# Kernel tuning notes

Measured on AMD Instinct MI355X. Metric: run time of the kernel, lower is better.

The kernel has to match this reference:

```python
import jax, jax.numpy as jnp
import numpy as np

K = 3        # kernel_size
GROUP = 32   # group
EPS = 1e-5   # BatchNorm eps


def setup_inputs() -> dict:
    key = jax.random.key(0)
    k1, k2 = jax.random.split(key)
    x = jax.random.normal(k1, (4, 256, 128, 128), jnp.float32)
    conv_w = jax.random.normal(k2, (GROUP * K * K, 256, K, K), jnp.float32) * 0.05
    gamma = jnp.ones((GROUP * K * K,), jnp.float32)
    beta = jnp.zeros((GROUP * K * K,), jnp.float32)
    return {"x": x, "conv_w": conv_w, "gamma": gamma, "beta": beta}


def _bilinear_align_corners(x, H, W):
    # F.upsample(..., mode='bilinear', align_corners=True)
    n, c, h, w = x.shape
    ys = jnp.linspace(0.0, h - 1.0, H)
    xs = jnp.linspace(0.0, w - 1.0, W)
    y0 = jnp.floor(ys).astype(jnp.int32)
    x0 = jnp.floor(xs).astype(jnp.int32)
    y1 = jnp.minimum(y0 + 1, h - 1)
    x1 = jnp.minimum(x0 + 1, w - 1)
    wy = (ys - y0)[None, None, :, None]
    wx = (xs - x0)[None, None, None, :]
    rows0 = x[:, :, y0, :]
    rows1 = x[:, :, y1, :]
    top = rows0[:, :, :, x0] * (1 - wx) + rows0[:, :, :, x1] * wx
    bot = rows1[:, :, :, x0] * (1 - wx) + rows1[:, :, :, x1] * wx
    return top * (1 - wy) + bot * wy


def reference(x, conv_w, gamma, beta):
    n, c, h0, w0 = x.shape
    # sigma = softmax(BN(conv(x))) over the full G*K*K channel dim
    sigma = jax.lax.conv_general_dilated(
        x, conv_w, (1, 1), 'VALID', dimension_numbers=('NCHW', 'OIHW', 'NCHW'))
    mean = sigma.mean(axis=(0, 2, 3))
    var = sigma.var(axis=(0, 2, 3))  # biased, matches BN training mode
    sigma = (sigma - mean[None, :, None, None]) * jax.lax.rsqrt(var + EPS)[None, :, None, None]
    sigma = sigma * gamma[None, :, None, None] + beta[None, :, None, None]
    sigma = jax.nn.softmax(sigma, axis=1)  # (n, G*K*K, h, w)
    h, w = sigma.shape[2], sigma.shape[3]  # h = h0-K+1, w = w0-K+1
    # Unfold: patches (n, c, K*K, h, w) with channel outer, kernel-pos inner (torch F.unfold order)
    patches = jnp.stack([x[:, :, i:i + h, j:j + w]
                         for i in range(K) for j in range(K)], axis=2)
    patches = patches.reshape(n, GROUP, c // GROUP, K * K, h, w)
    sig = sigma.reshape(n, GROUP, K * K, h, w)
    # Per-pixel, per-group weighted sum over the K*K window
    out = jnp.einsum('ngcphw,ngphw->ngchw', patches, sig).reshape(n, c, h, w)
    return _bilinear_align_corners(out, h0, w0)
```

## Files before the change

### kernel.cpp

```cpp
#include <hip/hip_runtime.h>
#include <hip/hip_bf16.h>
#include <math.h>

#define N 4
#define C 256
#define H 128
#define W 128
#define CO 288
#define OH 126
#define OW 126
#define GROUP 32
#define CPG 8
#define EPS 1e-5f

#define HW (OH*OW)
#define XSLICE (H*W)
#define XNSTRIDE (C*H*W)
#define SNSTRIDE (CO*HW)
#define LONSTRIDE (C*HW)
#define WSTRIDE (CO*256)
#define WTOT (9*CO*256)
#define XTOT (N*H*W*C)

typedef unsigned short u16;
typedef __attribute__((ext_vector_type(8))) short short8;
typedef __attribute__((ext_vector_type(4))) float float4v;

__device__ inline u16 f2bf(float v) {
    __hip_bfloat16 b = __float2bfloat16(v);
    return __builtin_bit_cast(u16, b);
}
__device__ inline float bf2f(u16 u) {
    __hip_bfloat16 b = __builtin_bit_cast(__hip_bfloat16, u);
    return __bfloat162float(b);
}

__global__ __launch_bounds__(256) void split_x_kernel(const float* __restrict__ x,
                                                      u16* __restrict__ xh,
                                                      u16* __restrict__ xl) {
    const int ci = threadIdx.x;
    const int w0 = blockIdx.x * 8;
    const int h  = blockIdx.y;
    const int n  = blockIdx.z;
    const float* src = x + ((size_t)(n*C + ci)*H + h)*W + w0;
    float4 v0 = *(const float4*)src;
    float4 v1 = *(const float4*)(src + 4);
    float vals[8] = {v0.x, v0.y, v0.z, v0.w, v1.x, v1.y, v1.z, v1.w};
    size_t obase = ((size_t)(n*H + h)*W + w0)*C + ci;
    #pragma unroll
    for (int dw = 0; dw < 8; ++dw) {
        float v = vals[dw];
        u16 hb = f2bf(v);
        xh[obase + (size_t)dw*C] = hb;
        xl[obase + (size_t)dw*C] = f2bf(v - bf2f(hb));
    }
}

__global__ __launch_bounds__(256) void split_w_kernel(const float* __restrict__ wgt,
                                                      u16* __restrict__ whT,
                                                      u16* __restrict__ wlT) {
    const int i = blockIdx.x*256 + threadIdx.x;
    const int ci = i & 255;
    const int co = (i >> 8) % CO;
    const int s  = i / (CO*256);
    float v = wgt[(size_t)co*(C*9) + (size_t)ci*9 + s];
    u16 hb = f2bf(v);
    whT[i] = hb;
    wlT[i] = f2bf(v - bf2f(hb));
}

__global__ __launch_bounds__(512, 2) void conv_mfma_kernel(const u16* __restrict__ xh,
                                                           const u16* __restrict__ whT,
                                                           float* __restrict__ sigma) {
    __shared__ __align__(16) u16 xs[25600];
    __shared__ __align__(16) u16 wsh[2*18432];

    const int tid  = threadIdx.x;
    const int wave = tid >> 6;
    const int lane = tid & 63;
    const int m16  = lane & 15;
    const int q    = lane >> 4;
    const int wr   = wave & 3;
    const int wc   = wave >> 2;
    const int ow0  = blockIdx.x * 64;
    const int oh0  = blockIdx.y * 4;
    const int n    = blockIdx.z;

    const int w_n    = (wave < 4) ? 5 : 4;
    const int w_base = (wave < 4) ? wave*320 : 1280 + (wave-4)*256;
    int wsrc[5];
    #pragma unroll
    for (int i = 0; i < 5; ++i) {
        int c = w_base + i*64 + lane;
        const int sp  = c / 1152;
        const int rem = c - sp*1152;
        const int qc  = rem / 288;
        const int co  = rem - qc*288;
        wsrc[i] = sp*WTOT + co*256 + qc*8;
    }

    int xoff[7];
    #pragma unroll
    for (int t = 0; t < 7; ++t) {
        int c = (8*t + wave)*64 + lane;
        if (c > 3167) c = 3167;
        const int spq = c / 396;
        const int rem = c - spq*396;
        const int row = rem / 66;
        const int col = rem - row*66;
        int gr = oh0 + row; if (gr > H-1) gr = H-1;
        int gc = ow0 + col; if (gc > W-1) gc = W-1;
        xoff[t] = (spq >> 2)*XTOT + ((n*H + gr)*W + gc)*C + (spq & 3)*8;
    }

    const int aoff = (q*396 + wr*66 + m16)*8;
    const int boff = (q*288 + wc*144 + m16)*8;

    float4v acc[4][9];
    #pragma unroll
    for (int mt = 0; mt < 4; ++mt)
        #pragma unroll
        for (int j = 0; j < 9; ++j) acc[mt][j] = (float4v)(0.f);

    #pragma unroll
    for (int t = 0; t < 7; ++t)
        if (t < 6 || wave < 2)
            __builtin_amdgcn_global_load_lds((const uint*)(xh + xoff[t]),
                                             (uint*)(xs + (8*t + wave)*512), 16, 0, 0);
    #pragma unroll
    for (int i = 0; i < 5; ++i)
        if (i < w_n)
            __builtin_amdgcn_global_load_lds((const uint*)(whT + wsrc[i]),
                                             (uint*)(wsh + (w_base + i*64)*8), 16, 0, 0);
    __syncthreads();

    int buf = 0;
    for (int ci0 = 0; ci0 < C; ci0 += 32) {
        #pragma unroll 1
        for (int s = 0; s < 9; ++s) {
            if (s < 8) {
                const int soff = (s+1)*WSTRIDE + ci0;
                #pragma unroll
                for (int i = 0; i < 5; ++i)
                    if (i < w_n)
                        __builtin_amdgcn_global_load_lds(
                            (const uint*)(whT + soff + wsrc[i]),
                            (uint*)(wsh + ((buf^1)*18432 + (w_base + i*64)*8)), 16, 0, 0);
            }

            const int ky = s / 3;
            const int kx = s - 3*ky;
            const int ab = aoff + (ky*66 + kx)*8;
            short8 ah0 = *(const short8*)&xs[ab];
            short8 ah1 = *(const short8*)&xs[ab + 128];
            short8 ah2 = *(const short8*)&xs[ab + 256];
            short8 ah3 = *(const short8*)&xs[ab + 384];
            short8 al0 = *(const short8*)&xs[ab + 12672];
            short8 al1 = *(const short8*)&xs[ab + 12672 + 128];
            short8 al2 = *(const short8*)&xs[ab + 12672 + 256];
            short8 al3 = *(const short8*)&xs[ab + 12672 + 384];

            if (s == 8) {
                __syncthreads();
                const int nci = ci0 + 32;
                if (nci < C) {
                    #pragma unroll
                    for (int t = 0; t < 7; ++t)
                        if (t < 6 || wave < 2)
                            __builtin_amdgcn_global_load_lds(
                                (const uint*)(xh + xoff[t] + nci),
                                (uint*)(xs + (8*t + wave)*512), 16, 0, 0);
                    #pragma unroll
                    for (int i = 0; i < 5; ++i)
                        if (i < w_n)
                            __builtin_amdgcn_global_load_lds(
                                (const uint*)(whT + nci + wsrc[i]),
                                (uint*)(wsh + ((buf^1)*18432 + (w_base + i*64)*8)), 16, 0, 0);
                }
            }

            const u16* wb = wsh + buf*18432 + boff;
            __builtin_amdgcn_s_setprio(1);
            #pragma unroll
            for (int j = 0; j < 9; ++j) {
                short8 bh = *(const short8*)&wb[j*128];
                acc[0][j] = __builtin_amdgcn_mfma_f32_16x16x32_bf16(ah0, bh, acc[0][j], 0, 0, 0);
                acc[1][j] = __builtin_amdgcn_mfma_f32_16x16x32_bf16(ah1, bh, acc[1][j], 0, 0, 0);
                acc[2][j] = __builtin_amdgcn_mfma_f32_16x16x32_bf16(ah2, bh, acc[2][j], 0, 0, 0);
                acc[3][j] = __builtin_amdgcn_mfma_f32_16x16x32_bf16(ah3, bh, acc[3][j], 0, 0, 0);
                acc[0][j] = __builtin_amdgcn_mfma_f32_16x16x32_bf16(al0, bh, acc[0][j], 0, 0, 0);
                acc[1][j] = __builtin_amdgcn_mfma_f32_16x16x32_bf16(al1, bh, acc[1][j], 0, 0, 0);
                acc[2][j] = __builtin_amdgcn_mfma_f32_16x16x32_bf16(al2, bh, acc[2][j], 0, 0, 0);
                acc[3][j] = __builtin_amdgcn_mfma_f32_16x16x32_bf16(al3, bh, acc[3][j], 0, 0, 0);
            }
            #pragma unroll
            for (int j = 0; j < 9; ++j) {
                short8 bl = *(const short8*)&wb[9216 + j*128];
                acc[0][j] = __builtin_amdgcn_mfma_f32_16x16x32_bf16(ah0, bl, acc[0][j], 0, 0, 0);
                acc[1][j] = __builtin_amdgcn_mfma_f32_16x16x32_bf16(ah1, bl, acc[1][j], 0, 0, 0);
                acc[2][j] = __builtin_amdgcn_mfma_f32_16x16x32_bf16(ah2, bl, acc[2][j], 0, 0, 0);
                acc[3][j] = __builtin_amdgcn_mfma_f32_16x16x32_bf16(ah3, bl, acc[3][j], 0, 0, 0);
            }
            __builtin_amdgcn_s_setprio(0);

            __syncthreads();
            buf ^= 1;
        }
    }

    const int oh = oh0 + wr;
    if (oh < OH) {
        #pragma unroll
        for (int mt = 0; mt < 4; ++mt) {
            const int posb = mt*16 + q*4;
            #pragma unroll
            for (int j = 0; j < 9; ++j) {
                const int co = wc*144 + j*16 + m16;
                float* dst = sigma + (size_t)n*SNSTRIDE + (size_t)co*HW + oh*OW;
                #pragma unroll
                for (int r = 0; r < 4; ++r) {
                    const int ow = ow0 + posb + r;
                    if (ow < OW) dst[ow] = acc[mt][j][r];
                }
            }
        }
    }
}

__global__ __launch_bounds__(1024) void stats_kernel(const float* __restrict__ sigma,
                                                     const float* __restrict__ gamma,
                                                     const float* __restrict__ beta,
                                                     float* __restrict__ coef) {
    const int c = blockIdx.x;
    float sum = 0.f, sq = 0.f;
    for (int n = 0; n < N; ++n) {
        const float* sp = sigma + (size_t)n*SNSTRIDE + (size_t)c*HW;
        for (int i = threadIdx.x; i < HW; i += 1024) {
            float v = sp[i];
            sum += v; sq += v * v;
        }
    }
    for (int off = 32; off > 0; off >>= 1) {
        sum += __shfl_down(sum, off, 64);
        sq  += __shfl_down(sq,  off, 64);
    }
    __shared__ float ls[16], lq[16];
    const int wid = threadIdx.x >> 6, lane = threadIdx.x & 63;
    if (lane == 0) { ls[wid] = sum; lq[wid] = sq; }
    __syncthreads();
    if (threadIdx.x == 0) {
        float S = 0.f, Q = 0.f;
        #pragma unroll
        for (int i = 0; i < 16; ++i) { S += ls[i]; Q += lq[i]; }
        const float cnt = (float)(N * HW);
        float mean = S / cnt;
        float var  = Q / cnt - mean * mean;
        float a = gamma[c] * rsqrtf(var + EPS);
        coef[c]      = a;
        coef[CO + c] = beta[c] - mean * a;
    }
}

__global__ __launch_bounds__(256) void fuse_kernel(const float* __restrict__ x,
                                                   const float* __restrict__ sigma,
                                                   const float* __restrict__ coef,
                                                   float* __restrict__ outlo,
                                                   float* __restrict__ sums) {
    __shared__ float a[CO], b[CO];
    for (int i = threadIdx.x; i < CO; i += 256) {
        a[i] = coef[i];
        b[i] = coef[CO + i];
    }
    __syncthreads();

    const int t4 = blockIdx.x * 256 + threadIdx.x;
    if (t4 >= N * HW * 4) return;
    const int gpos = t4 >> 2;
    const int gc   = t4 & 3;
    const int n  = gpos / HW;
    const int hw = gpos - n * HW;
    const int oh = hw / OW;
    const int ow = hw - oh * OW;

    const float* sp = sigma + (size_t)n * SNSTRIDE + hw;
    const float* xb = x + (size_t)n * XNSTRIDE + oh * W + ow;
    float* ob = outlo + (size_t)n * LONSTRIDE + hw;

    float sum = 0.f;
    for (int gl = 0; gl < 8; ++gl) {
        const int g = gc * 8 + gl;
        float acc[CPG];
        #pragma unroll
        for (int c = 0; c < CPG; ++c) acc[c] = 0.f;
        #pragma unroll
        for (int p = 0; p < 9; ++p) {
            const int ch = g * 9 + p;
            float s = sp[(size_t)ch * HW] * a[ch] + b[ch];
            float e = __expf(s);
            sum += e;
            const float* xr = xb + (size_t)(g * CPG) * XSLICE + (p / 3) * W + (p % 3);
            #pragma unroll
            for (int c = 0; c < CPG; ++c)
                acc[c] += xr[(size_t)c * XSLICE] * e;
        }
        #pragma unroll
        for (int c = 0; c < CPG; ++c)
            ob[(size_t)(g * CPG + c) * HW] = acc[c];
    }
    sum += __shfl_xor(sum, 1, 64);
    sum += __shfl_xor(sum, 2, 64);
    if (gc == 0) sums[gpos] = sum;
}

__global__ __launch_bounds__(256) void upsample_kernel(const float* __restrict__ lo,
                                                       const float* __restrict__ sums,
                                                       float* __restrict__ out) {
    const int idx = blockIdx.x * 256 + threadIdx.x;
    const int xi = idx & (W - 1);
    const int yi = (idx >> 7) & (H - 1);
    const int nc = idx >> 14;
    const int n  = nc >> 8;

    const float scale = 125.0f / 127.0f;
    const float sy = yi * scale;
    const float sx = xi * scale;
    int y0 = (int)sy;
    int x0 = (int)sx;
    float wy = sy - (float)y0;
    float wx = sx - (float)x0;
    int y1 = min(y0 + 1, OH - 1);
    int x1 = min(x0 + 1, OW - 1);

    const float* p  = lo + (size_t)nc * HW;
    const float* ps = sums + (size_t)n * HW;
    float v00 = p[y0 * OW + x0] / ps[y0 * OW + x0];
    float v01 = p[y0 * OW + x1] / ps[y0 * OW + x1];
    float v10 = p[y1 * OW + x0] / ps[y1 * OW + x0];
    float v11 = p[y1 * OW + x1] / ps[y1 * OW + x1];
    float top = v00 * (1.f - wx) + v01 * wx;
    float bot = v10 * (1.f - wx) + v11 * wx;
    out[idx] = top * (1.f - wy) + bot * wy;
}

extern "C" void kernel_launch(void* const* d_in, const int* in_sizes, int n_in,
                              void* d_out, int out_size, void* d_ws, size_t ws_size,
                              hipStream_t stream) {
    const float* x      = (const float*)d_in[0];
    const float* conv_w = (const float*)d_in[1];
    const float* gamma  = (const float*)d_in[2];
    const float* beta   = (const float*)d_in[3];
    float* out = (float*)d_out;
    float* ws  = (float*)d_ws;

    float* sigma = ws;
    float* coef  = ws + 18289152;
    float* outlo = ws + 18290176;
    u16* xhp = (u16*)(ws + 18290176);
    u16* xlp = xhp + (size_t)XTOT;
    u16* whT = xlp + (size_t)XTOT;
    u16* wlT = whT + (size_t)WTOT;
    float* sums = (float*)whT;

    split_x_kernel<<<dim3(16, 128, 4), 256, 0, stream>>>(x, xhp, xlp);
    split_w_kernel<<<(9*CO*256)/256, 256, 0, stream>>>(conv_w, whT, wlT);

    conv_mfma_kernel<<<dim3(2, 32, N), 512, 0, stream>>>(xhp, whT, sigma);

    stats_kernel<<<CO, 1024, 0, stream>>>(sigma, gamma, beta, coef);

    fuse_kernel<<<(N * HW * 4 + 255) / 256, 256, 0, stream>>>(x, sigma, coef, outlo, sums);

    upsample_kernel<<<(N * C * H * W) / 256, 256, 0, stream>>>(outlo, sums, out);
}
```

Baseline: 596.3 us.

## Stage input rows in double-buffered shared memory for the fuse kernel

The fuse kernel now uses one 512-thread block per output row. For each group it stages the eight channels' three input rows in shared memory, double-buffered so the next group's rows load while the current group computes. Each thread now covers all 32 groups but only two channels per group, so the 3x3 window reuse comes from shared memory instead of repeated global or cache reads. In exchange, each softmax exponential is computed four times, once per channel-pair thread, and a block barrier is added for every group.

Result: faster. 550.5 us (median of 2 runs) (-7.7%).

```diff
diff --git a/kernel.cpp b/kernel.cpp
--- a/kernel.cpp
+++ b/kernel.cpp
@@ -261,55 +261,81 @@
     }
 }
 
-__global__ __launch_bounds__(256) void fuse_kernel(const float* __restrict__ x,
+__global__ __launch_bounds__(512) void fuse_kernel(const float* __restrict__ x,
                                                    const float* __restrict__ sigma,
                                                    const float* __restrict__ coef,
                                                    float* __restrict__ outlo,
                                                    float* __restrict__ sums) {
     __shared__ float a[CO], b[CO];
-    for (int i = threadIdx.x; i < CO; i += 256) {
+    __shared__ float xbuf[2][8*3*128];
+
+    const int tid = threadIdx.x;
+    for (int i = tid; i < CO; i += 512) {
         a[i] = coef[i];
         b[i] = coef[CO + i];
     }
+
+    const int oh = blockIdx.x % OH;
+    const int n  = blockIdx.x / OH;
+    const float* xrow = x + (size_t)n * XNSTRIDE + (size_t)oh * W;
+
+    const int f0row = tid >> 5, f0w4 = tid & 31;
+    const int f1row = (512 + tid) >> 5, f1w4 = tid & 31;
+
+    const int pos = tid >> 2;
+    const int gc  = tid & 3;
+    const bool act = pos < OW;
+    const int hw = oh * OW + pos;
+    const float* sp = sigma + (size_t)n * SNSTRIDE + hw;
+    float* ob = outlo + (size_t)n * LONSTRIDE + hw;
+
+    {
+        const float* src = xrow;
+        const int ch = f0row / 3, r = f0row - 3*ch;
+        *(float4*)&xbuf[0][f0row*128 + f0w4*4] =
+            *(const float4*)(src + (size_t)ch*XSLICE + r*W + f0w4*4);
+        if (tid < 256) {
+            const int ch1 = f1row / 3, r1 = f1row - 3*ch1;
+            *(float4*)&xbuf[0][f1row*128 + f1w4*4] =
+                *(const float4*)(src + (size_t)ch1*XSLICE + r1*W + f1w4*4);
+        }
+    }
     __syncthreads();
 
-    const int t4 = blockIdx.x * 256 + threadIdx.x;
-    if (t4 >= N * HW * 4) return;
-    const int gpos = t4 >> 2;
-    const int gc   = t4 & 3;
-    const int n  = gpos / HW;
-    const int hw = gpos - n * HW;
-    const int oh = hw / OW;
-    const int ow = hw - oh * OW;
-
-    const float* sp = sigma + (size_t)n * SNSTRIDE + hw;
-    const float* xb = x + (size_t)n * XNSTRIDE + oh * W + ow;
-    float* ob = outlo + (size_t)n * LONSTRIDE + hw;
-
     float sum = 0.f;
-    for (int gl = 0; gl < 8; ++gl) {
-        const int g = gc * 8 + gl;
-        float acc[CPG];
-        #pragma unroll
-        for (int c = 0; c < CPG; ++c) acc[c] = 0.f;
-        #pragma unroll
-        for (int p = 0; p < 9; ++p) {
-            const int ch = g * 9 + p;
-            float s = sp[(size_t)ch * HW] * a[ch] + b[ch];
-            float e = __expf(s);
-            sum += e;
-            const float* xr = xb + (size_t)(g * CPG) * XSLICE + (p / 3) * W + (p % 3);
+    int buf = 0;
+    for (int g = 0; g < GROUP; ++g) {
+        if (g + 1 < GROUP) {
+            const float* src = xrow + (size_t)((g+1)*CPG)*XSLICE;
+            const int ch = f0row / 3, r = f0row - 3*ch;
+            *(float4*)&xbuf[buf^1][f0row*128 + f0w4*4] =
+                *(const float4*)(src + (size_t)ch*XSLICE + r*W + f0w4*4);
+            if (tid < 256) {
+                const int ch1 = f1row / 3, r1 = f1row - 3*ch1;
+                *(float4*)&xbuf[buf^1][f1row*128 + f1w4*4] =
+                    *(const float4*)(src + (size_t)ch1*XSLICE + r1*W + f1w4*4);
+            }
+        }
+        if (act) {
+            float acc0 = 0.f, acc1 = 0.f;
             #pragma unroll
-            for (int c = 0; c < CPG; ++c)
-                acc[c] += xr[(size_t)c * XSLICE] * e;
-        }
-        #pragma unroll
-        for (int c = 0; c < CPG; ++c)
-            ob[(size_t)(g * CPG + c) * HW] = acc[c];
-    }
-    sum += __shfl_xor(sum, 1, 64);
-    sum += __shfl_xor(sum, 2, 64);
-    if (gc == 0) sums[gpos] = sum;
+            for (int p = 0; p < 9; ++p) {
+                const int ch = g * 9 + p;
+                float s = sp[(size_t)ch * HW] * a[ch] + b[ch];
+                float e = __expf(s);
+                sum += e;
+                const int r = p / 3, cx = p - 3*r;
+                const int w = pos + cx;
+                acc0 += xbuf[buf][((gc*2 + 0)*3 + r)*128 + w] * e;
+                acc1 += xbuf[buf][((gc*2 + 1)*3 + r)*128 + w] * e;
+            }
+            ob[(size_t)(g*CPG + gc*2 + 0) * HW] = acc0;
+            ob[(size_t)(g*CPG + gc*2 + 1) * HW] = acc1;
+        }
+        __syncthreads();
+        buf ^= 1;
+    }
+    if (act && gc == 0) sums[(size_t)n * HW + hw] = sum;
 }
 
 __global__ __launch_bounds__(256) void upsample_kernel(const float* __restrict__ lo,
@@ -368,7 +394,7 @@
 
     stats_kernel<<<CO, 1024, 0, stream>>>(sigma, gamma, beta, coef);
 
-    fuse_kernel<<<(N * HW * 4 + 255) / 256, 256, 0, stream>>>(x, sigma, coef, outlo, sums);
+    fuse_kernel<<<N * OH, 512, 0, stream>>>(x, sigma, coef, outlo, sums);
 
     upsample_kernel<<<(N * C * H * W) / 256, 256, 0, stream>>>(outlo, sums, out);
 }
```
